# Kernel tuning notes

Measured on AMD Instinct MI355X. Metric: run time of the kernel, lower is better.

Reference implementation:

```python
import jax, jax.numpy as jnp
import numpy as np

N, E = 50000, 1250000
IN_DIM, H, C, EDGE_DIM = 128, 2, 32, 64
NEG_SLOPE = 0.2


def setup_inputs() -> dict:
    key = jax.random.key(0)
    ks = jax.random.split(key, 9)
    x = jax.random.normal(ks[0], (N, IN_DIM), dtype=jnp.float32)
    edge_index = jax.random.randint(ks[1], (2, E), 0, N, dtype=jnp.int64)
    edge_attr = jax.random.normal(ks[2], (E, EDGE_DIM), dtype=jnp.float32)
    # learned params (PyG GATConv: glorot-style scale)
    W = jax.random.normal(ks[3], (IN_DIM, H * C), dtype=jnp.float32) * (1.0 / np.sqrt(IN_DIM))
    W_edge = jax.random.normal(ks[4], (EDGE_DIM, H * C), dtype=jnp.float32) * (1.0 / np.sqrt(EDGE_DIM))
    att_src = jax.random.normal(ks[5], (H, C), dtype=jnp.float32) * (1.0 / np.sqrt(C))
    att_dst = jax.random.normal(ks[6], (H, C), dtype=jnp.float32) * (1.0 / np.sqrt(C))
    att_edge = jax.random.normal(ks[7], (H, C), dtype=jnp.float32) * (1.0 / np.sqrt(C))
    bias = jnp.zeros((H * C,), dtype=jnp.float32)
    return {"x": x, "edge_index": edge_index, "edge_attr": edge_attr,
            "W": W, "W_edge": W_edge, "att_src": att_src, "att_dst": att_dst,
            "att_edge": att_edge, "bias": bias}


def reference(x, edge_index, edge_attr, W, W_edge, att_src, att_dst, att_edge, bias):
    # IntraGraphAttention.forward: relu then GATConv(in, 32, heads=2, edge_dim=64)
    x = jax.nn.relu(x)
    src, dst = edge_index[0], edge_index[1]

    # PyG add_self_loops(fill_value='mean'): self-loop edge_attr = mean of
    # incoming edge attrs per node (zeros for isolated nodes).
    deg = jax.ops.segment_sum(jnp.ones((E,), jnp.float32), dst, num_segments=N)
    loop_attr = jax.ops.segment_sum(edge_attr, dst, num_segments=N) / jnp.maximum(deg, 1.0)[:, None]
    loop_idx = jnp.arange(N, dtype=src.dtype)
    src_f = jnp.concatenate([src, loop_idx])          # [E+N]
    dst_f = jnp.concatenate([dst, loop_idx])          # [E+N]
    eattr_f = jnp.concatenate([edge_attr, loop_attr])  # [E+N, 64]

    # node / edge projections
    h = (x @ W).reshape(N, H, C)                       # [N,H,C]
    a_src = jnp.einsum('nhc,hc->nh', h, att_src)       # [N,H]
    a_dst = jnp.einsum('nhc,hc->nh', h, att_dst)       # [N,H]
    e = (eattr_f @ W_edge).reshape(-1, H, C)           # [E+N,H,C]
    a_edge = jnp.einsum('ehc,hc->eh', e, att_edge)     # [E+N,H]

    # per-edge attention logits
    alpha = a_src[src_f] + a_dst[dst_f] + a_edge       # [E+N,H]
    alpha = jax.nn.leaky_relu(alpha, NEG_SLOPE)

    # segment softmax over destination neighborhoods
    amax = jax.ops.segment_max(alpha, dst_f, num_segments=N)  # [N,H]
    p = jnp.exp(alpha - amax[dst_f])
    denom = jax.ops.segment_sum(p, dst_f, num_segments=N)     # [N,H]
    alpha = p / (denom[dst_f] + 1e-16)

    # scatter-aggregate messages (dropout dp=0 -> identity)
    msg = h[src_f] * alpha[..., None]                   # [E+N,H,C]
    out = jax.ops.segment_sum(msg, dst_f, num_segments=N)     # [N,H,C]
    return out.reshape(N, H * C) + bias
```

## Files before the change

### kernel.cpp

```cpp
#include <hip/hip_runtime.h>

#define NEG 0.2f

__global__ __launch_bounds__(256) void k_zero(int* __restrict__ p, int n) {
    int i = blockIdx.x * 256 + threadIdx.x;
    if (i < n) p[i] = 0;
}

__global__ __launch_bounds__(256) void k_node(
    const float* __restrict__ x, const float* __restrict__ W,
    const float* __restrict__ att_src, const float* __restrict__ att_dst,
    float* __restrict__ hbuf, float* __restrict__ a_src, float* __restrict__ a_dst, int N) {
    __shared__ float Wl[128 * 64];
    __shared__ float xs[4 * 128];
    int t = threadIdx.x;
    for (int i = t; i < 128 * 64; i += 256) Wl[i] = W[i];
    int col = t & 63;
    int nl  = t >> 6;
    float asw = att_src[col];
    float adw = att_dst[col];
    int node0 = blockIdx.x * 64;
    __syncthreads();
    for (int it = 0; it < 16; ++it) {
        int nb = node0 + it * 4;
        __syncthreads();
        for (int j = t; j < 512; j += 256) {
            int nn = nb + (j >> 7);
            int k  = j & 127;
            xs[j] = (nn < N) ? fmaxf(x[(size_t)nn * 128 + k], 0.f) : 0.f;
        }
        __syncthreads();
        int n = nb + nl;
        float acc = 0.f;
#pragma unroll 8
        for (int k = 0; k < 128; ++k)
            acc = fmaf(xs[nl * 128 + k], Wl[k * 64 + col], acc);
        float vs = acc * asw, vd = acc * adw;
#pragma unroll
        for (int m = 1; m <= 16; m <<= 1) {
            vs += __shfl_xor(vs, m, 64);
            vd += __shfl_xor(vd, m, 64);
        }
        if (n < N) {
            hbuf[(size_t)n * 64 + col] = acc;
            if ((col & 31) == 0) {
                int hh = col >> 5;
                a_src[n * 2 + hh] = vs;
                a_dst[n * 2 + hh] = vd;
            }
        }
    }
}

__global__ __launch_bounds__(256) void k_hist(
    const int* __restrict__ dstI, int* __restrict__ count, long long E,
    const float* __restrict__ W_edge, const float* __restrict__ att_edge,
    float* __restrict__ wke) {
    if (blockIdx.x == 0 && threadIdx.x < 128) {
        int hh = threadIdx.x >> 6;
        int k  = threadIdx.x & 63;
        float s = 0.f;
#pragma unroll
        for (int c = 0; c < 32; ++c)
            s += W_edge[k * 64 + hh * 32 + c] * att_edge[hh * 32 + c];
        wke[hh * 64 + k] = s;
    }
    long long i0 = (long long)blockIdx.x * 256 + threadIdx.x;
    long long stride = (long long)gridDim.x * 256;
    for (long long i = i0; i < E; i += stride)
        atomicAdd(&count[dstI[i]], 1);
}

__global__ __launch_bounds__(256) void k_scan1(const int* __restrict__ cnt, int* __restrict__ offs,
                                               int* __restrict__ bsum, int N) {
    __shared__ int ts[256];
    int t = threadIdx.x, blk = blockIdx.x;
    int base = blk * 1024 + t * 4;
    int v[4], s = 0;
#pragma unroll
    for (int i = 0; i < 4; ++i) {
        int idx = base + i;
        v[i] = (idx < N) ? cnt[idx] : 0;
        s += v[i];
    }
    ts[t] = s;
    __syncthreads();
    for (int off = 1; off < 256; off <<= 1) {
        int y = (t >= off) ? ts[t - off] : 0;
        __syncthreads();
        ts[t] += y;
        __syncthreads();
    }
    int run = ts[t] - s;
#pragma unroll
    for (int i = 0; i < 4; ++i) {
        int idx = base + i;
        if (idx < N) offs[idx] = run;
        run += v[i];
    }
    if (t == 255) bsum[blk] = ts[255];
}

__global__ void k_scan2(int* __restrict__ bsum, int nb) {
    int t = threadIdx.x;
    int orig = (t < nb) ? bsum[t] : 0;
    int v = orig;
#pragma unroll
    for (int off = 1; off < 64; off <<= 1) {
        int y = __shfl_up(v, off, 64);
        if (t >= off) v += y;
    }
    if (t < nb) bsum[t] = v - orig;
}

__global__ void k_scan3(int* __restrict__ offs, const int* __restrict__ bsum,
                        int* __restrict__ cursor, int N) {
    int idx = blockIdx.x * 256 + threadIdx.x;
    if (idx < N) {
        int o = offs[idx] + bsum[idx >> 10];
        offs[idx] = o;
        cursor[idx] = o;
    }
}

__global__ __launch_bounds__(256) void k_pa(
    const float* __restrict__ edge_attr, const int* __restrict__ srcI,
    const int* __restrict__ dstI, const float* __restrict__ wke,
    int* __restrict__ cursor, float4* __restrict__ evec, long long E) {
    __shared__ float wkes[128];
    if (threadIdx.x < 128) wkes[threadIdx.x] = wke[threadIdx.x];
    __syncthreads();
    long long i0 = (long long)blockIdx.x * 256 + threadIdx.x;
    long long stride = (long long)gridDim.x * 256;
    for (long long e = i0; e < E; e += stride) {
        const float4* row = (const float4*)(edge_attr + e * 64);
        float pa0 = 0.f, pa1 = 0.f;
#pragma unroll
        for (int k = 0; k < 16; ++k) {
            float4 ea = row[k];
            float4 wa = *(const float4*)(wkes + k * 4);
            float4 wb = *(const float4*)(wkes + 64 + k * 4);
            pa0 += ea.x * wa.x + ea.y * wa.y + ea.z * wa.z + ea.w * wa.w;
            pa1 += ea.x * wb.x + ea.y * wb.y + ea.z * wb.z + ea.w * wb.w;
        }
        int s = srcI[e], d = dstI[e];
        int pos = atomicAdd(&cursor[d], 1);
        evec[pos] = make_float4(pa0, pa1, __int_as_float(s), 0.f);
    }
}

__global__ __launch_bounds__(256) void k_agg(
    const float4* __restrict__ evec, const int* __restrict__ offs,
    const int* __restrict__ count, const float* __restrict__ a_src,
    const float* __restrict__ a_dst, const float* __restrict__ hbuf,
    const float* __restrict__ bias, float* __restrict__ out, int N) {
    int t = threadIdx.x;
    int lane = t & 63;
    int sub = lane & 15;
    int grp = lane >> 4;
    int n = blockIdx.x * 4 + (t >> 6);
    if (n >= N) return;
    int cnt  = count[n];
    int base = offs[n];
    float ad0 = a_dst[n * 2 + 0], ad1 = a_dst[n * 2 + 1];
    float accx = 0.f, accy = 0.f, accz = 0.f, accw = 0.f;
    float den0 = 0.f, den1 = 0.f, sae0 = 0.f, sae1 = 0.f;

    if (cnt > 0) {
        int last = cnt - 1;
        float4 evA = evec[base + (grp < cnt ? grp : last)];
        float4 evB = evec[base + (grp + 4 < cnt ? grp + 4 : last)];
        int sA = __float_as_int(evA.z);
        int sB = __float_as_int(evB.z);
        float2 asA = *(const float2*)(a_src + 2 * (size_t)sA);
        float4 hvA = *(const float4*)(hbuf + (size_t)sA * 64 + sub * 4);
        for (int j = grp; j < cnt; j += 4) {
            int jc = j + 8 < cnt ? j + 8 : last;
            float4 evC = evec[base + jc];
            float2 asB = *(const float2*)(a_src + 2 * (size_t)sB);
            float4 hvB = *(const float4*)(hbuf + (size_t)sB * 64 + sub * 4);
            float l0 = asA.x + ad0 + evA.x; l0 = l0 > 0.f ? l0 : NEG * l0;
            float l1 = asA.y + ad1 + evA.y; l1 = l1 > 0.f ? l1 : NEG * l1;
            float q0 = __expf(l0), q1 = __expf(l1);
            float q = (sub < 8) ? q0 : q1;
            accx = fmaf(q, hvA.x, accx);
            accy = fmaf(q, hvA.y, accy);
            accz = fmaf(q, hvA.z, accz);
            accw = fmaf(q, hvA.w, accw);
            den0 += q0; den1 += q1;
            sae0 += evA.x; sae1 += evA.y;
            evA = evB; sA = sB; asA = asB; hvA = hvB;
            evB = evC; sB = __float_as_int(evC.z);
        }
    }
#define RED2(v) { v += __shfl_xor(v, 16, 64); v += __shfl_xor(v, 32, 64); }
    RED2(accx) RED2(accy) RED2(accz) RED2(accw)
    RED2(den0) RED2(den1) RED2(sae0) RED2(sae1)
#undef RED2

    float dg = (cnt > 0) ? (float)cnt : 1.f;
    float as0 = a_src[n * 2 + 0], as1 = a_src[n * 2 + 1];
    float l0 = as0 + ad0 + sae0 / dg; l0 = l0 > 0.f ? l0 : NEG * l0;
    float l1 = as1 + ad1 + sae1 / dg; l1 = l1 > 0.f ? l1 : NEG * l1;
    float pl0 = __expf(l0), pl1 = __expf(l1);
    const float4 hn = *(const float4*)(hbuf + (size_t)n * 64 + sub * 4);
    float pl  = (sub < 8) ? pl0 : pl1;
    float den = ((sub < 8) ? den0 + pl0 : den1 + pl1) + 1e-16f;
    const float4 bv = *(const float4*)(bias + sub * 4);
    if (grp == 0) {
        float4 o;
        o.x = (accx + pl * hn.x) / den + bv.x;
        o.y = (accy + pl * hn.y) / den + bv.y;
        o.z = (accz + pl * hn.z) / den + bv.z;
        o.w = (accw + pl * hn.w) / den + bv.w;
        *(float4*)(out + (size_t)n * 64 + sub * 4) = o;
    }
}

extern "C" void kernel_launch(void* const* d_in, const int* in_sizes, int n_in,
                              void* d_out, int out_size, void* d_ws, size_t ws_size,
                              hipStream_t stream) {
    const float* x         = (const float*)d_in[0];
    const int*   ei        = (const int*)d_in[1];
    const float* edge_attr = (const float*)d_in[2];
    const float* W         = (const float*)d_in[3];
    const float* W_edge    = (const float*)d_in[4];
    const float* att_src   = (const float*)d_in[5];
    const float* att_dst   = (const float*)d_in[6];
    const float* att_edge  = (const float*)d_in[7];
    const float* bias      = (const float*)d_in[8];

    int N = in_sizes[0] / 128;
    long long E = in_sizes[1] / 2;
    const int* srcI = ei;
    const int* dstI = ei + E;

    char* ws = (char*)d_ws;
    float4* evec  = (float4*)ws;                      ws += (size_t)E * 16;
    float* wke    = (float*)ws;                       ws += 128 * 4;
    float* hbuf   = (float*)ws;                       ws += (size_t)N * 64 * 4;
    float* a_src  = (float*)ws;                       ws += (size_t)N * 2 * 4;
    float* a_dst  = (float*)ws;                       ws += (size_t)N * 2 * 4;
    int*   count  = (int*)ws;                         ws += (size_t)N * 4;
    int*   offs   = (int*)ws;                         ws += (size_t)N * 4;
    int*   cursor = (int*)ws;                         ws += (size_t)N * 4;
    int*   bsum   = (int*)ws;                         ws += 64 * 4;

    k_zero<<<(N + 255) / 256, 256, 0, stream>>>(count, N);
    k_node<<<(N + 63) / 64, 256, 0, stream>>>(x, W, att_src, att_dst, hbuf, a_src, a_dst, N);
    k_hist<<<2048, 256, 0, stream>>>(dstI, count, E, W_edge, att_edge, wke);

    int nb = (N + 1023) / 1024;
    k_scan1<<<nb, 256, 0, stream>>>(count, offs, bsum, N);
    k_scan2<<<1, 64, 0, stream>>>(bsum, nb);
    k_scan3<<<(N + 255) / 256, 256, 0, stream>>>(offs, bsum, cursor, N);

    k_pa<<<2048, 256, 0, stream>>>(edge_attr, srcI, dstI, wke, cursor, evec, E);

    k_agg<<<(N + 3) / 4, 256, 0, stream>>>(evec, offs, count, a_src, a_dst, hbuf, bias,
                                           (float*)d_out, N);
}
```

Before: 297.5 us.

## Fuse all pipeline stages into one persistent cooperative kernel with grid syncs

```diff
diff --git a/kernel.cpp b/kernel.cpp
--- a/kernel.cpp
+++ b/kernel.cpp
@@ -1,262 +1,264 @@
 #include <hip/hip_runtime.h>
+#include <hip/hip_cooperative_groups.h>
 
 #define NEG 0.2f
 
-__global__ __launch_bounds__(256) void k_zero(int* __restrict__ p, int n) {
-    int i = blockIdx.x * 256 + threadIdx.x;
-    if (i < n) p[i] = 0;
-}
-
-__global__ __launch_bounds__(256) void k_node(
-    const float* __restrict__ x, const float* __restrict__ W,
-    const float* __restrict__ att_src, const float* __restrict__ att_dst,
-    float* __restrict__ hbuf, float* __restrict__ a_src, float* __restrict__ a_dst, int N) {
+namespace cg = cooperative_groups;
+
+struct Args {
+    const float* x; const int* srcI; const int* dstI; const float* edge_attr;
+    const float* W; const float* W_edge; const float* att_src; const float* att_dst;
+    const float* att_edge; const float* bias;
+    float* wke; float* hbuf; float* a_src; float* a_dst;
+    int* count; int* offs; int* cursor; int* bsum;
+    float4* evec; float* out;
+    int N; long long E;
+};
+
+__global__ __launch_bounds__(256, 4) void fused(Args a) {
     __shared__ float Wl[128 * 64];
-    __shared__ float xs[4 * 128];
-    int t = threadIdx.x;
-    for (int i = t; i < 128 * 64; i += 256) Wl[i] = W[i];
-    int col = t & 63;
-    int nl  = t >> 6;
-    float asw = att_src[col];
-    float adw = att_dst[col];
-    int node0 = blockIdx.x * 64;
-    __syncthreads();
-    for (int it = 0; it < 16; ++it) {
-        int nb = node0 + it * 4;
-        __syncthreads();
-        for (int j = t; j < 512; j += 256) {
-            int nn = nb + (j >> 7);
-            int k  = j & 127;
-            xs[j] = (nn < N) ? fmaxf(x[(size_t)nn * 128 + k], 0.f) : 0.f;
-        }
-        __syncthreads();
-        int n = nb + nl;
-        float acc = 0.f;
-#pragma unroll 8
-        for (int k = 0; k < 128; ++k)
-            acc = fmaf(xs[nl * 128 + k], Wl[k * 64 + col], acc);
-        float vs = acc * asw, vd = acc * adw;
-#pragma unroll
-        for (int m = 1; m <= 16; m <<= 1) {
-            vs += __shfl_xor(vs, m, 64);
-            vd += __shfl_xor(vd, m, 64);
-        }
-        if (n < N) {
-            hbuf[(size_t)n * 64 + col] = acc;
-            if ((col & 31) == 0) {
-                int hh = col >> 5;
-                a_src[n * 2 + hh] = vs;
-                a_dst[n * 2 + hh] = vd;
-            }
-        }
-    }
-}
-
-__global__ __launch_bounds__(256) void k_hist(
-    const int* __restrict__ dstI, int* __restrict__ count, long long E,
-    const float* __restrict__ W_edge, const float* __restrict__ att_edge,
-    float* __restrict__ wke) {
-    if (blockIdx.x == 0 && threadIdx.x < 128) {
-        int hh = threadIdx.x >> 6;
-        int k  = threadIdx.x & 63;
+    __shared__ float xs[512];
+    cg::grid_group grid = cg::this_grid();
+    const int t   = threadIdx.x;
+    const int NB  = gridDim.x;
+    const long long gtid    = (long long)blockIdx.x * 256 + t;
+    const long long gstride = (long long)NB * 256;
+    const int N = a.N;
+    const long long E = a.E;
+
+    for (long long i = gtid; i < N; i += gstride) a.count[i] = 0;
+    if (blockIdx.x == 0 && t < 128) {
+        int hh = t >> 6, k = t & 63;
         float s = 0.f;
 #pragma unroll
         for (int c = 0; c < 32; ++c)
-            s += W_edge[k * 64 + hh * 32 + c] * att_edge[hh * 32 + c];
-        wke[hh * 64 + k] = s;
-    }
-    long long i0 = (long long)blockIdx.x * 256 + threadIdx.x;
-    long long stride = (long long)gridDim.x * 256;
-    for (long long i = i0; i < E; i += stride)
-        atomicAdd(&count[dstI[i]], 1);
-}
-
-__global__ __launch_bounds__(256) void k_scan1(const int* __restrict__ cnt, int* __restrict__ offs,
-                                               int* __restrict__ bsum, int N) {
-    __shared__ int ts[256];
-    int t = threadIdx.x, blk = blockIdx.x;
-    int base = blk * 1024 + t * 4;
-    int v[4], s = 0;
+            s += a.W_edge[k * 64 + hh * 32 + c] * a.att_edge[hh * 32 + c];
+        a.wke[hh * 64 + k] = s;
+    }
+    {
+        for (int i = t; i < 128 * 64; i += 256) Wl[i] = a.W[i];
+        int col = t & 63;
+        int nl  = t >> 6;
+        float asw = a.att_src[col];
+        float adw = a.att_dst[col];
+        __syncthreads();
+        int ngroups = (N + 63) / 64;
+        for (int g = blockIdx.x; g < ngroups; g += NB) {
+            int node0 = g * 64;
+            for (int it = 0; it < 16; ++it) {
+                int nb = node0 + it * 4;
+                __syncthreads();
+                for (int j = t; j < 512; j += 256) {
+                    int nn = nb + (j >> 7);
+                    int k  = j & 127;
+                    xs[j] = (nn < N) ? fmaxf(a.x[(size_t)nn * 128 + k], 0.f) : 0.f;
+                }
+                __syncthreads();
+                int n = nb + nl;
+                float acc = 0.f;
+#pragma unroll 8
+                for (int k = 0; k < 128; ++k)
+                    acc = fmaf(xs[nl * 128 + k], Wl[k * 64 + col], acc);
+                float vs = acc * asw, vd = acc * adw;
 #pragma unroll
-    for (int i = 0; i < 4; ++i) {
-        int idx = base + i;
-        v[i] = (idx < N) ? cnt[idx] : 0;
-        s += v[i];
-    }
-    ts[t] = s;
-    __syncthreads();
-    for (int off = 1; off < 256; off <<= 1) {
-        int y = (t >= off) ? ts[t - off] : 0;
-        __syncthreads();
-        ts[t] += y;
-        __syncthreads();
-    }
-    int run = ts[t] - s;
+                for (int m = 1; m <= 16; m <<= 1) {
+                    vs += __shfl_xor(vs, m, 64);
+                    vd += __shfl_xor(vd, m, 64);
+                }
+                if (n < N) {
+                    a.hbuf[(size_t)n * 64 + col] = acc;
+                    if ((col & 31) == 0) {
+                        int hh = col >> 5;
+                        a.a_src[n * 2 + hh] = vs;
+                        a.a_dst[n * 2 + hh] = vd;
+                    }
+                }
+            }
+        }
+    }
+    grid.sync();
+
+    for (long long i = gtid; i < E; i += gstride)
+        atomicAdd(&a.count[a.dstI[i]], 1);
+    grid.sync();
+
+    const int PB = (N + NB - 1) / NB;
+    int* ts = (int*)xs;
+    {
+        int base = blockIdx.x * PB;
+        int v = 0;
+        if (t < PB && base + t < N) v = a.count[base + t];
+        ts[t] = v;
+        __syncthreads();
+        for (int off = 1; off < 256; off <<= 1) {
+            int y = (t >= off) ? ts[t - off] : 0;
+            __syncthreads();
+            ts[t] += y;
+            __syncthreads();
+        }
+        int incl = ts[t];
+        if (t < PB && base + t < N) a.offs[base + t] = incl - v;
+        if (t == 255) a.bsum[blockIdx.x] = ts[255];
+    }
+    grid.sync();
+
+    if (blockIdx.x == 0) {
+        int K = (NB + 255) / 256;
+        int vloc[4]; int s = 0;
+        for (int i = 0; i < K; ++i) {
+            int idx = t * K + i;
+            vloc[i] = (idx < NB) ? a.bsum[idx] : 0;
+            s += vloc[i];
+        }
+        ts[t] = s;
+        __syncthreads();
+        for (int off = 1; off < 256; off <<= 1) {
+            int y = (t >= off) ? ts[t - off] : 0;
+            __syncthreads();
+            ts[t] += y;
+            __syncthreads();
+        }
+        int run = ts[t] - s;
+        for (int i = 0; i < K; ++i) {
+            int idx = t * K + i;
+            if (idx < NB) a.bsum[idx] = run;
+            run += vloc[i];
+        }
+    }
+    grid.sync();
+
+    for (long long i = gtid; i < N; i += gstride) {
+        int o = a.offs[i] + a.bsum[(int)(i / PB)];
+        a.offs[i] = o;
+        a.cursor[i] = o;
+    }
+    grid.sync();
+
+    {
+        float* wkes = xs;
+        if (t < 128) wkes[t] = a.wke[t];
+        __syncthreads();
+        for (long long e = gtid; e < E; e += gstride) {
+            const float4* row = (const float4*)(a.edge_attr + e * 64);
+            float pa0 = 0.f, pa1 = 0.f;
 #pragma unroll
-    for (int i = 0; i < 4; ++i) {
-        int idx = base + i;
-        if (idx < N) offs[idx] = run;
-        run += v[i];
-    }
-    if (t == 255) bsum[blk] = ts[255];
-}
-
-__global__ void k_scan2(int* __restrict__ bsum, int nb) {
-    int t = threadIdx.x;
-    int orig = (t < nb) ? bsum[t] : 0;
-    int v = orig;
-#pragma unroll
-    for (int off = 1; off < 64; off <<= 1) {
-        int y = __shfl_up(v, off, 64);
-        if (t >= off) v += y;
-    }
-    if (t < nb) bsum[t] = v - orig;
-}
-
-__global__ void k_scan3(int* __restrict__ offs, const int* __restrict__ bsum,
-                        int* __restrict__ cursor, int N) {
-    int idx = blockIdx.x * 256 + threadIdx.x;
-    if (idx < N) {
-        int o = offs[idx] + bsum[idx >> 10];
-        offs[idx] = o;
-        cursor[idx] = o;
-    }
-}
-
-__global__ __launch_bounds__(256) void k_pa(
-    const float* __restrict__ edge_attr, const int* __restrict__ srcI,
-    const int* __restrict__ dstI, const float* __restrict__ wke,
-    int* __restrict__ cursor, float4* __restrict__ evec, long long E) {
-    __shared__ float wkes[128];
-    if (threadIdx.x < 128) wkes[threadIdx.x] = wke[threadIdx.x];
-    __syncthreads();
-    long long i0 = (long long)blockIdx.x * 256 + threadIdx.x;
-    long long stride = (long long)gridDim.x * 256;
-    for (long long e = i0; e < E; e += stride) {
-        const float4* row = (const float4*)(edge_attr + e * 64);
-        float pa0 = 0.f, pa1 = 0.f;
-#pragma unroll
-        for (int k = 0; k < 16; ++k) {
-            float4 ea = row[k];
-            float4 wa = *(const float4*)(wkes + k * 4);
-            float4 wb = *(const float4*)(wkes + 64 + k * 4);
-            pa0 += ea.x * wa.x + ea.y * wa.y + ea.z * wa.z + ea.w * wa.w;
-            pa1 += ea.x * wb.x + ea.y * wb.y + ea.z * wb.z + ea.w * wb.w;
-        }
-        int s = srcI[e], d = dstI[e];
-        int pos = atomicAdd(&cursor[d], 1);
-        evec[pos] = make_float4(pa0, pa1, __int_as_float(s), 0.f);
-    }
-}
-
-__global__ __launch_bounds__(256) void k_agg(
-    const float4* __restrict__ evec, const int* __restrict__ offs,
-    const int* __restrict__ count, const float* __restrict__ a_src,
-    const float* __restrict__ a_dst, const float* __restrict__ hbuf,
-    const float* __restrict__ bias, float* __restrict__ out, int N) {
-    int t = threadIdx.x;
-    int lane = t & 63;
-    int sub = lane & 15;
-    int grp = lane >> 4;
-    int n = blockIdx.x * 4 + (t >> 6);
-    if (n >= N) return;
-    int cnt  = count[n];
-    int base = offs[n];
-    float ad0 = a_dst[n * 2 + 0], ad1 = a_dst[n * 2 + 1];
-    float accx = 0.f, accy = 0.f, accz = 0.f, accw = 0.f;
-    float den0 = 0.f, den1 = 0.f, sae0 = 0.f, sae1 = 0.f;
-
-    if (cnt > 0) {
-        int last = cnt - 1;
-        float4 evA = evec[base + (grp < cnt ? grp : last)];
-        float4 evB = evec[base + (grp + 4 < cnt ? grp + 4 : last)];
-        int sA = __float_as_int(evA.z);
-        int sB = __float_as_int(evB.z);
-        float2 asA = *(const float2*)(a_src + 2 * (size_t)sA);
-        float4 hvA = *(const float4*)(hbuf + (size_t)sA * 64 + sub * 4);
-        for (int j = grp; j < cnt; j += 4) {
-            int jc = j + 8 < cnt ? j + 8 : last;
-            float4 evC = evec[base + jc];
-            float2 asB = *(const float2*)(a_src + 2 * (size_t)sB);
-            float4 hvB = *(const float4*)(hbuf + (size_t)sB * 64 + sub * 4);
-            float l0 = asA.x + ad0 + evA.x; l0 = l0 > 0.f ? l0 : NEG * l0;
-            float l1 = asA.y + ad1 + evA.y; l1 = l1 > 0.f ? l1 : NEG * l1;
-            float q0 = __expf(l0), q1 = __expf(l1);
-            float q = (sub < 8) ? q0 : q1;
-            accx = fmaf(q, hvA.x, accx);
-            accy = fmaf(q, hvA.y, accy);
-            accz = fmaf(q, hvA.z, accz);
-            accw = fmaf(q, hvA.w, accw);
-            den0 += q0; den1 += q1;
-            sae0 += evA.x; sae1 += evA.y;
-            evA = evB; sA = sB; asA = asB; hvA = hvB;
-            evB = evC; sB = __float_as_int(evC.z);
-        }
-    }
+            for (int k = 0; k < 16; ++k) {
+                float4 ea = row[k];
+                float4 wa = *(const float4*)(wkes + k * 4);
+                float4 wb = *(const float4*)(wkes + 64 + k * 4);
+                pa0 += ea.x * wa.x + ea.y * wa.y + ea.z * wa.z + ea.w * wa.w;
+                pa1 += ea.x * wb.x + ea.y * wb.y + ea.z * wb.z + ea.w * wb.w;
+            }
+            int s = a.srcI[e], d = a.dstI[e];
+            int pos = atomicAdd(&a.cursor[d], 1);
+            a.evec[pos] = make_float4(pa0, pa1, __int_as_float(s), 0.f);
+        }
+    }
+    grid.sync();
+
+    {
+        int lane = t & 63;
+        int sub = lane & 15;
+        int grp = lane >> 4;
+        int ngroups = (N + 3) / 4;
+        for (int g = blockIdx.x; g < ngroups; g += NB) {
+            int n = g * 4 + (t >> 6);
+            if (n >= N) continue;
+            int cnt  = a.count[n];
+            int base = a.offs[n];
+            float ad0 = a.a_dst[n * 2 + 0], ad1 = a.a_dst[n * 2 + 1];
+            float accx = 0.f, accy = 0.f, accz = 0.f, accw = 0.f;
+            float den0 = 0.f, den1 = 0.f, sae0 = 0.f, sae1 = 0.f;
+            if (cnt > 0) {
+                int last = cnt - 1;
+                float4 evA = a.evec[base + (grp < cnt ? grp : last)];
+                float4 evB = a.evec[base + (grp + 4 < cnt ? grp + 4 : last)];
+                int sA = __float_as_int(evA.z);
+                int sB = __float_as_int(evB.z);
+                float2 asA = *(const float2*)(a.a_src + 2 * (size_t)sA);
+                float4 hvA = *(const float4*)(a.hbuf + (size_t)sA * 64 + sub * 4);
+                for (int j = grp; j < cnt; j += 4) {
+                    int jc = j + 8 < cnt ? j + 8 : last;
+                    float4 evC = a.evec[base + jc];
+                    float2 asB = *(const float2*)(a.a_src + 2 * (size_t)sB);
+                    float4 hvB = *(const float4*)(a.hbuf + (size_t)sB * 64 + sub * 4);
+                    float l0 = asA.x + ad0 + evA.x; l0 = l0 > 0.f ? l0 : NEG * l0;
+                    float l1 = asA.y + ad1 + evA.y; l1 = l1 > 0.f ? l1 : NEG * l1;
+                    float q0 = __expf(l0), q1 = __expf(l1);
+                    float q = (sub < 8) ? q0 : q1;
+                    accx = fmaf(q, hvA.x, accx);
+                    accy = fmaf(q, hvA.y, accy);
+                    accz = fmaf(q, hvA.z, accz);
+                    accw = fmaf(q, hvA.w, accw);
+                    den0 += q0; den1 += q1;
+                    sae0 += evA.x; sae1 += evA.y;
+                    evA = evB; sA = sB; asA = asB; hvA = hvB;
+                    evB = evC; sB = __float_as_int(evC.z);
+                }
+            }
 #define RED2(v) { v += __shfl_xor(v, 16, 64); v += __shfl_xor(v, 32, 64); }
-    RED2(accx) RED2(accy) RED2(accz) RED2(accw)
-    RED2(den0) RED2(den1) RED2(sae0) RED2(sae1)
+            RED2(accx) RED2(accy) RED2(accz) RED2(accw)
+            RED2(den0) RED2(den1) RED2(sae0) RED2(sae1)
 #undef RED2
-
-    float dg = (cnt > 0) ? (float)cnt : 1.f;
-    float as0 = a_src[n * 2 + 0], as1 = a_src[n * 2 + 1];
-    float l0 = as0 + ad0 + sae0 / dg; l0 = l0 > 0.f ? l0 : NEG * l0;
-    float l1 = as1 + ad1 + sae1 / dg; l1 = l1 > 0.f ? l1 : NEG * l1;
-    float pl0 = __expf(l0), pl1 = __expf(l1);
-    const float4 hn = *(const float4*)(hbuf + (size_t)n * 64 + sub * 4);
-    float pl  = (sub < 8) ? pl0 : pl1;
-    float den = ((sub < 8) ? den0 + pl0 : den1 + pl1) + 1e-16f;
-    const float4 bv = *(const float4*)(bias + sub * 4);
-    if (grp == 0) {
-        float4 o;
-        o.x = (accx + pl * hn.x) / den + bv.x;
-        o.y = (accy + pl * hn.y) / den + bv.y;
-        o.z = (accz + pl * hn.z) / den + bv.z;
-        o.w = (accw + pl * hn.w) / den + bv.w;
-        *(float4*)(out + (size_t)n * 64 + sub * 4) = o;
+            float dg = (cnt > 0) ? (float)cnt : 1.f;
+            float as0 = a.a_src[n * 2 + 0], as1 = a.a_src[n * 2 + 1];
+            float l0 = as0 + ad0 + sae0 / dg; l0 = l0 > 0.f ? l0 : NEG * l0;
+            float l1 = as1 + ad1 + sae1 / dg; l1 = l1 > 0.f ? l1 : NEG * l1;
+            float pl0 = __expf(l0), pl1 = __expf(l1);
+            const float4 hn = *(const float4*)(a.hbuf + (size_t)n * 64 + sub * 4);
+            float pl  = (sub < 8) ? pl0 : pl1;
+            float den = ((sub < 8) ? den0 + pl0 : den1 + pl1) + 1e-16f;
+            const float4 bv = *(const float4*)(a.bias + sub * 4);
+            if (grp == 0) {
+                float4 o;
+                o.x = (accx + pl * hn.x) / den + bv.x;
+                o.y = (accy + pl * hn.y) / den + bv.y;
+                o.z = (accz + pl * hn.z) / den + bv.z;
+                o.w = (accw + pl * hn.w) / den + bv.w;
+                *(float4*)(a.out + (size_t)n * 64 + sub * 4) = o;
+            }
+        }
     }
 }
 
 extern "C" void kernel_launch(void* const* d_in, const int* in_sizes, int n_in,
                               void* d_out, int out_size, void* d_ws, size_t ws_size,
                               hipStream_t stream) {
-    const float* x         = (const float*)d_in[0];
-    const int*   ei        = (const int*)d_in[1];
-    const float* edge_attr = (const float*)d_in[2];
-    const float* W         = (const float*)d_in[3];
-    const float* W_edge    = (const float*)d_in[4];
-    const float* att_src   = (const float*)d_in[5];
-    const float* att_dst   = (const float*)d_in[6];
-    const float* att_edge  = (const float*)d_in[7];
-    const float* bias      = (const float*)d_in[8];
-
-    int N = in_sizes[0] / 128;
-    long long E = in_sizes[1] / 2;
-    const int* srcI = ei;
-    const int* dstI = ei + E;
+    Args a;
+    a.x         = (const float*)d_in[0];
+    const int* ei = (const int*)d_in[1];
+    a.edge_attr = (const float*)d_in[2];
+    a.W         = (const float*)d_in[3];
+    a.W_edge    = (const float*)d_in[4];
+    a.att_src   = (const float*)d_in[5];
+    a.att_dst   = (const float*)d_in[6];
+    a.att_edge  = (const float*)d_in[7];
+    a.bias      = (const float*)d_in[8];
+    a.N = in_sizes[0] / 128;
+    a.E = in_sizes[1] / 2;
+    a.srcI = ei;
+    a.dstI = ei + a.E;
+    a.out  = (float*)d_out;
 
     char* ws = (char*)d_ws;
-    float4* evec  = (float4*)ws;                      ws += (size_t)E * 16;
-    float* wke    = (float*)ws;                       ws += 128 * 4;
-    float* hbuf   = (float*)ws;                       ws += (size_t)N * 64 * 4;
-    float* a_src  = (float*)ws;                       ws += (size_t)N * 2 * 4;
-    float* a_dst  = (float*)ws;                       ws += (size_t)N * 2 * 4;
-    int*   count  = (int*)ws;                         ws += (size_t)N * 4;
-    int*   offs   = (int*)ws;                         ws += (size_t)N * 4;
-    int*   cursor = (int*)ws;                         ws += (size_t)N * 4;
-    int*   bsum   = (int*)ws;                         ws += 64 * 4;
-
-    k_zero<<<(N + 255) / 256, 256, 0, stream>>>(count, N);
-    k_node<<<(N + 63) / 64, 256, 0, stream>>>(x, W, att_src, att_dst, hbuf, a_src, a_dst, N);
-    k_hist<<<2048, 256, 0, stream>>>(dstI, count, E, W_edge, att_edge, wke);
-
-    int nb = (N + 1023) / 1024;
-    k_scan1<<<nb, 256, 0, stream>>>(count, offs, bsum, N);
-    k_scan2<<<1, 64, 0, stream>>>(bsum, nb);
-    k_scan3<<<(N + 255) / 256, 256, 0, stream>>>(offs, bsum, cursor, N);
-
-    k_pa<<<2048, 256, 0, stream>>>(edge_attr, srcI, dstI, wke, cursor, evec, E);
-
-    k_agg<<<(N + 3) / 4, 256, 0, stream>>>(evec, offs, count, a_src, a_dst, hbuf, bias,
-                                           (float*)d_out, N);
+    a.evec   = (float4*)ws;             ws += (size_t)a.E * 16;
+    a.wke    = (float*)ws;              ws += 128 * 4;
+    a.hbuf   = (float*)ws;              ws += (size_t)a.N * 64 * 4;
+    a.a_src  = (float*)ws;              ws += (size_t)a.N * 2 * 4;
+    a.a_dst  = (float*)ws;              ws += (size_t)a.N * 2 * 4;
+    a.count  = (int*)ws;                ws += (size_t)a.N * 4;
+    a.offs   = (int*)ws;                ws += (size_t)a.N * 4;
+    a.cursor = (int*)ws;                ws += (size_t)a.N * 4;
+    a.bsum   = (int*)ws;                ws += 2048 * 4;
+
+    int maxb = 0;
+    if (hipOccupancyMaxActiveBlocksPerMultiprocessor(
+            &maxb, reinterpret_cast<const void*>(&fused), 256, 0) != hipSuccess || maxb <= 0)
+        maxb = 4;
+    int NB = maxb * 256;
+    if (NB > 1024) NB = 1024;
+
+    void* params[] = { &a };
+    hipLaunchCooperativeKernel(reinterpret_cast<const void*>(&fused),
+                               dim3(NB), dim3(256), params, 0, stream);
 }
```

Result: slower. 778.7 us (+161.7%).

## Register-tile node projection GEMM with 4x4 per-thread outer products

Applied to the files above, without the earlier changes.

```diff
diff --git a/kernel.cpp b/kernel.cpp
--- a/kernel.cpp
+++ b/kernel.cpp
@@ -7,47 +7,62 @@
     if (i < n) p[i] = 0;
 }
 
-__global__ __launch_bounds__(256) void k_node(
+__global__ __launch_bounds__(128) void k_node(
     const float* __restrict__ x, const float* __restrict__ W,
     const float* __restrict__ att_src, const float* __restrict__ att_dst,
     float* __restrict__ hbuf, float* __restrict__ a_src, float* __restrict__ a_dst, int N) {
+    __shared__ float xs[128 * 36];
     __shared__ float Wl[128 * 64];
-    __shared__ float xs[4 * 128];
-    int t = threadIdx.x;
-    for (int i = t; i < 128 * 64; i += 256) Wl[i] = W[i];
-    int col = t & 63;
-    int nl  = t >> 6;
-    float asw = att_src[col];
-    float adw = att_dst[col];
-    int node0 = blockIdx.x * 64;
+    const int t  = threadIdx.x;
+    const int tn = t & 7;
+    const int tc = t >> 3;
+    const int node0 = blockIdx.x * 32;
+
+    for (int j = t; j < 128 * 64; j += 128) Wl[j] = W[j];
+    for (int j = t; j < 32 * 128; j += 128) {
+        int n = j >> 7, k = j & 127;
+        int nn = node0 + n;
+        xs[k * 36 + n] = (nn < N) ? fmaxf(x[(size_t)nn * 128 + k], 0.f) : 0.f;
+    }
     __syncthreads();
-    for (int it = 0; it < 16; ++it) {
-        int nb = node0 + it * 4;
-        __syncthreads();
-        for (int j = t; j < 512; j += 256) {
-            int nn = nb + (j >> 7);
-            int k  = j & 127;
-            xs[j] = (nn < N) ? fmaxf(x[(size_t)nn * 128 + k], 0.f) : 0.f;
-        }
-        __syncthreads();
-        int n = nb + nl;
-        float acc = 0.f;
+
+    float4 acc[4] = {{0,0,0,0},{0,0,0,0},{0,0,0,0},{0,0,0,0}};
 #pragma unroll 8
-        for (int k = 0; k < 128; ++k)
-            acc = fmaf(xs[nl * 128 + k], Wl[k * 64 + col], acc);
-        float vs = acc * asw, vd = acc * adw;
-#pragma unroll
-        for (int m = 1; m <= 16; m <<= 1) {
+    for (int k = 0; k < 128; ++k) {
+        const float4 xv = *(const float4*)(xs + k * 36 + 4 * tn);
+        const float4 wv = *(const float4*)(Wl + k * 64 + 4 * tc);
+        acc[0].x = fmaf(xv.x, wv.x, acc[0].x); acc[0].y = fmaf(xv.x, wv.y, acc[0].y);
+        acc[0].z = fmaf(xv.x, wv.z, acc[0].z); acc[0].w = fmaf(xv.x, wv.w, acc[0].w);
+        acc[1].x = fmaf(xv.y, wv.x, acc[1].x); acc[1].y = fmaf(xv.y, wv.y, acc[1].y);
+        acc[1].z = fmaf(xv.y, wv.z, acc[1].z); acc[1].w = fmaf(xv.y, wv.w, acc[1].w);
+        acc[2].x = fmaf(xv.z, wv.x, acc[2].x); acc[2].y = fmaf(xv.z, wv.y, acc[2].y);
+        acc[2].z = fmaf(xv.z, wv.z, acc[2].z); acc[2].w = fmaf(xv.z, wv.w, acc[2].w);
+        acc[3].x = fmaf(xv.w, wv.x, acc[3].x); acc[3].y = fmaf(xv.w, wv.y, acc[3].y);
+        acc[3].z = fmaf(xv.w, wv.z, acc[3].z); acc[3].w = fmaf(xv.w, wv.w, acc[3].w);
+    }
+
+#pragma unroll
+    for (int n = 0; n < 4; ++n) {
+        int nn = node0 + 4 * tn + n;
+        if (nn < N) *(float4*)(hbuf + (size_t)nn * 64 + 4 * tc) = acc[n];
+    }
+
+    const float4 as4 = *(const float4*)(att_src + 4 * tc);
+    const float4 ad4 = *(const float4*)(att_dst + 4 * tc);
+    int head = (t >= 64) ? 1 : 0;
+#pragma unroll
+    for (int n = 0; n < 4; ++n) {
+        float vs = acc[n].x * as4.x + acc[n].y * as4.y + acc[n].z * as4.z + acc[n].w * as4.w;
+        float vd = acc[n].x * ad4.x + acc[n].y * ad4.y + acc[n].z * ad4.z + acc[n].w * ad4.w;
+#pragma unroll
+        for (int m = 8; m <= 32; m <<= 1) {
             vs += __shfl_xor(vs, m, 64);
             vd += __shfl_xor(vd, m, 64);
         }
-        if (n < N) {
-            hbuf[(size_t)n * 64 + col] = acc;
-            if ((col & 31) == 0) {
-                int hh = col >> 5;
-                a_src[n * 2 + hh] = vs;
-                a_dst[n * 2 + hh] = vd;
-            }
+        int nn = node0 + 4 * tn + n;
+        if ((t & 63) < 8 && nn < N) {
+            a_src[nn * 2 + head] = vs;
+            a_dst[nn * 2 + head] = vd;
         }
     }
 }
@@ -247,7 +262,7 @@
     int*   bsum   = (int*)ws;                         ws += 64 * 4;
 
     k_zero<<<(N + 255) / 256, 256, 0, stream>>>(count, N);
-    k_node<<<(N + 63) / 64, 256, 0, stream>>>(x, W, att_src, att_dst, hbuf, a_src, a_dst, N);
+    k_node<<<(N + 31) / 32, 128, 0, stream>>>(x, W, att_src, att_dst, hbuf, a_src, a_dst, N);
     k_hist<<<2048, 256, 0, stream>>>(dstI, count, E, W_edge, att_edge, wke);
 
     int nb = (N + 1023) / 1024;
```

New measurement: 295.5 us. About the same (-0.7%).
